# Performance work log

Hardware: AMD Instinct MI355X
Metric: run time of the kernel (lower is better)

Reference implementation:

```python
import jax, jax.numpy as jnp
import numpy as np

N = 50000
IN_DIM = 512
HID = 8
HEADS = 8
OUT_DIM = 7
E = 1600000
NEG_SLOPE = 0.2  # PyG GATConv default leaky_relu slope


def setup_inputs() -> dict:
    key = jax.random.key(0)
    ks = jax.random.split(key, 12)
    x = jax.random.normal(ks[0], (N, IN_DIM), dtype=jnp.float32)
    edge_index = jax.random.randint(ks[1], (2, E), 0, N, dtype=jnp.int64)
    s1 = 1.0 / np.sqrt(IN_DIM)
    s2 = 1.0 / np.sqrt(HID * HEADS)
    W1 = jax.random.normal(ks[2], (IN_DIM, HEADS * HID), dtype=jnp.float32) * s1
    att_src1 = jax.random.normal(ks[3], (HEADS, HID), dtype=jnp.float32) * s1
    att_dst1 = jax.random.normal(ks[4], (HEADS, HID), dtype=jnp.float32) * s1
    b1 = jnp.zeros((HEADS * HID,), dtype=jnp.float32)
    W2 = jax.random.normal(ks[5], (HEADS * HID, OUT_DIM), dtype=jnp.float32) * s2
    att_src2 = jax.random.normal(ks[6], (1, OUT_DIM), dtype=jnp.float32) * s2
    att_dst2 = jax.random.normal(ks[7], (1, OUT_DIM), dtype=jnp.float32) * s2
    b2 = jnp.zeros((OUT_DIM,), dtype=jnp.float32)
    return {"x": x, "edge_index": edge_index, "W1": W1, "att_src1": att_src1,
            "att_dst1": att_dst1, "b1": b1, "W2": W2, "att_src2": att_src2,
            "att_dst2": att_dst2, "b2": b2}


def _gat_layer(x, W, a_src, a_dst, b, src, dst, heads, out_ch, concat):
    n = x.shape[0]
    h = (x @ W).reshape(n, heads, out_ch)            # [N,H,C]
    asrc = jnp.sum(h * a_src, axis=-1)               # [N,H]
    adst = jnp.sum(h * a_dst, axis=-1)               # [N,H]
    e = jax.nn.leaky_relu(asrc[src] + adst[dst], NEG_SLOPE)   # [E,H]
    m = jax.ops.segment_max(e, dst, num_segments=n)           # segment softmax (stable)
    ex = jnp.exp(e - m[dst])
    s = jax.ops.segment_sum(ex, dst, num_segments=n)
    alpha = ex / jnp.maximum(s[dst], 1e-16)                   # [E,H]
    out = jax.ops.segment_sum(h[src] * alpha[..., None], dst, num_segments=n)  # [N,H,C]
    out = out.reshape(n, heads * out_ch) if concat else out.mean(axis=1)
    return out + b


def reference(x, edge_index, W1, att_src1, att_dst1, b1, W2, att_src2, att_dst2, b2):
    # add self-loops (PyG GATConv default add_self_loops=True)
    loop = jnp.arange(N, dtype=edge_index.dtype)
    src = jnp.concatenate([edge_index[0], loop])
    dst = jnp.concatenate([edge_index[1], loop])
    h = _gat_layer(x, W1, att_src1, att_dst1, b1, src, dst, HEADS, HID, True)
    h = jax.nn.elu(h)
    # dropout is identity at inference
    logits = _gat_layer(h, W2, att_src2, att_dst2, b2, src, dst, 1, OUT_DIM, False)
    return logits
```

## Files before the change

kernel.cpp:

```cpp
#include <hip/hip_runtime.h>
#include <hip/hip_bf16.h>

#define IN_DIM 512
#define HEADS 8
#define HID 8
#define OUT_DIM 7
#define NEG_SLOPE 0.2f

typedef __attribute__((ext_vector_type(8))) short short8b;
typedef __attribute__((ext_vector_type(4))) float f32x4;

#define BSHIFT 7
#define BMASK 127
#define K3_EPT 16

__device__ __forceinline__ unsigned short f2bf_rne(float f) {
    unsigned u = __float_as_uint(f);
    unsigned r = (u + 0x7FFFu + ((u >> 16) & 1u)) >> 16;
    return (unsigned short)r;
}
__device__ __forceinline__ float bf2f(unsigned short s) {
    return __uint_as_float((unsigned)s << 16);
}

__global__ __launch_bounds__(256) void prep_kernel(
    const float* __restrict__ W1, unsigned short* __restrict__ bhi,
    unsigned short* __restrict__ blo,
    const int* __restrict__ dst, int* __restrict__ bucketCounts, int E, int nbuck)
{
    __shared__ int cnt[512];
    int t = threadIdx.x;
    if (blockIdx.x < 128) {
        int i = blockIdx.x * 256 + t;
        int j = i & 7;
        int lane = (i >> 3) & 63;
        int T = (i >> 9) & 3;
        int chunk = i >> 11;
        int col = 16 * T + (lane & 15);
        int k = chunk * 32 + 8 * (lane >> 4) + j;
        float w = W1[k * 64 + col];
        unsigned u = __float_as_uint(w);
        unsigned hu = u & 0xFFFF0000u;
        float rem = w - __uint_as_float(hu);
        bhi[i] = (unsigned short)(hu >> 16);
        blo[i] = (unsigned short)(__float_as_uint(rem) >> 16);
    } else {
        int b = blockIdx.x - 128;
        cnt[t] = 0; cnt[t + 256] = 0;
        __syncthreads();
        int i = b * 256 + t;
        int stride = 512 * 256;
        for (; i < E; i += stride) atomicAdd(&cnt[dst[i] >> BSHIFT], 1);
        __syncthreads();
        if (t < nbuck && cnt[t]) atomicAdd(&bucketCounts[t], cnt[t]);
        int t2 = t + 256;
        if (t2 < nbuck && cnt[t2]) atomicAdd(&bucketCounts[t2], cnt[t2]);
    }
}

__global__ __launch_bounds__(512) void bucket_scan_kernel(
    const int* __restrict__ bucketCounts, int* __restrict__ bucketBase,
    int* __restrict__ bucketCursor, int nbuck)
{
    __shared__ int wsum[8];
    int t = threadIdx.x, lane = t & 63, w = t >> 6;
    int c = (t < nbuck) ? bucketCounts[t] : 0;
    int inc = c;
    #pragma unroll
    for (int d = 1; d < 64; d <<= 1) {
        int u = __shfl_up(inc, d);
        if (lane >= d) inc += u;
    }
    if (lane == 63) wsum[w] = inc;
    __syncthreads();
    if (t == 0) { int run = 0; for (int k = 0; k < 8; ++k) { int tmp = wsum[k]; wsum[k] = run; run += tmp; } }
    __syncthreads();
    int excl = inc - c + wsum[w];
    if (t < nbuck) { bucketBase[t] = excl; bucketCursor[t] = excl; }
    if (t == nbuck) bucketBase[t] = excl;
}

__global__ __launch_bounds__(256) void gemm1_coarse_kernel(
    const float* __restrict__ x,
    const unsigned short* __restrict__ bhi, const unsigned short* __restrict__ blo,
    const float* __restrict__ as1, const float* __restrict__ ad1,
    unsigned short* __restrict__ h1, float* __restrict__ asrc1, float* __restrict__ adst1,
    int n,
    const int* __restrict__ src, const int* __restrict__ dstv,
    int* __restrict__ bucketCursor, unsigned int* __restrict__ tmp, int E, int nGemm)
{
    __shared__ float lds[4][32][68];
    int t = threadIdx.x;

    if ((int)blockIdx.x >= nGemm) {
        int* cnt   = (int*)&lds[0][0][0];
        int* gbase = cnt + 512;
        cnt[t] = 0; cnt[t + 256] = 0;
        __syncthreads();
        int base = (blockIdx.x - nGemm) * (256 * K3_EPT);
        unsigned int pk[K3_EPT];
        unsigned int meta[K3_EPT];
        #pragma unroll
        for (int j = 0; j < K3_EPT; ++j) {
            int i = base + t + j * 256;
            if (i < E) {
                int d = dstv[i], s = src[i];
                int b = d >> BSHIFT;
                pk[j] = ((unsigned)s << 16) | (unsigned)(d & BMASK);
                int r = atomicAdd(&cnt[b], 1);
                meta[j] = ((unsigned)r << 9) | (unsigned)b;
            } else {
                meta[j] = 0xFFFFFFFFu; pk[j] = 0;
            }
        }
        __syncthreads();
        if (cnt[t] > 0) gbase[t] = atomicAdd(&bucketCursor[t], cnt[t]);
        int t2 = t + 256;
        if (cnt[t2] > 0) gbase[t2] = atomicAdd(&bucketCursor[t2], cnt[t2]);
        __syncthreads();
        #pragma unroll
        for (int j = 0; j < K3_EPT; ++j) {
            if (meta[j] != 0xFFFFFFFFu) {
                int b = meta[j] & 511;
                int r = meta[j] >> 9;
                tmp[gbase[b] + r] = pk[j];
            }
        }
        return;
    }

    int wave = t >> 6, l = t & 63;
    int il = l & 15, g = l >> 4;
    int r0 = blockIdx.x * 32;
    int kw = wave * 128;

    f32x4 acc[2][4] = {{{0.f,0.f,0.f,0.f},{0.f,0.f,0.f,0.f},{0.f,0.f,0.f,0.f},{0.f,0.f,0.f,0.f}},
                       {{0.f,0.f,0.f,0.f},{0.f,0.f,0.f,0.f},{0.f,0.f,0.f,0.f},{0.f,0.f,0.f,0.f}}};

    #pragma unroll
    for (int ph = 0; ph < 2; ++ph) {
        #pragma unroll
        for (int j = 0; j < 8; ++j) {
            int idx = j * 64 + l;
            int row = idx >> 4;
            int kq = idx & 15;
            int gr = r0 + row; if (gr >= n) gr = n - 1;
            float4 v = *(const float4*)(x + (size_t)gr * IN_DIM + kw + ph * 64 + kq * 4);
            *(float4*)(&lds[wave][row][kq * 4]) = v;
        }
        #pragma unroll
        for (int itp = 0; itp < 2; ++itp) {
            int it = ph * 2 + itp;
            int chunk = wave * 4 + it;
            const short8b* bh = (const short8b*)bhi + (size_t)(chunk * 4) * 64 + l;
            const short8b* bl = (const short8b*)blo + (size_t)(chunk * 4) * 64 + l;
            short8b Bh[4], Bl[4];
            #pragma unroll
            for (int T = 0; T < 4; ++T) { Bh[T] = bh[T * 64]; Bl[T] = bl[T * 64]; }
            #pragma unroll
            for (int rg = 0; rg < 2; ++rg) {
                float av[8];
                *(float4*)(&av[0]) = *(const float4*)(&lds[wave][rg * 16 + il][32 * itp + 8 * g]);
                *(float4*)(&av[4]) = *(const float4*)(&lds[wave][rg * 16 + il][32 * itp + 8 * g + 4]);
                short8b Ahi, Alo;
                #pragma unroll
                for (int j = 0; j < 8; ++j) {
                    unsigned u = __float_as_uint(av[j]);
                    unsigned hu = u & 0xFFFF0000u;
                    float rem = av[j] - __uint_as_float(hu);
                    Ahi[j] = (short)(hu >> 16);
                    Alo[j] = (short)(__float_as_uint(rem) >> 16);
                }
                #pragma unroll
                for (int T = 0; T < 4; ++T) {
                    acc[rg][T] = __builtin_amdgcn_mfma_f32_16x16x32_bf16(Alo, Bh[T], acc[rg][T], 0, 0, 0);
                    acc[rg][T] = __builtin_amdgcn_mfma_f32_16x16x32_bf16(Ahi, Bl[T], acc[rg][T], 0, 0, 0);
                    acc[rg][T] = __builtin_amdgcn_mfma_f32_16x16x32_bf16(Ahi, Bh[T], acc[rg][T], 0, 0, 0);
                }
            }
        }
    }

    #pragma unroll
    for (int rg = 0; rg < 2; ++rg)
        #pragma unroll
        for (int T = 0; T < 4; ++T)
            #pragma unroll
            for (int r = 0; r < 4; ++r)
                lds[wave][rg * 16 + 4 * g + r][16 * T + il] = acc[rg][T][r];
    __syncthreads();

    #pragma unroll
    for (int half = 0; half < 2; ++half) {
        int i = t + half * 256;
        int row = i >> 4, c0 = (i & 15) * 4;
        int grow = r0 + row;
        float v0 = lds[0][row][c0]     + lds[1][row][c0]     + lds[2][row][c0]     + lds[3][row][c0];
        float v1 = lds[0][row][c0 + 1] + lds[1][row][c0 + 1] + lds[2][row][c0 + 1] + lds[3][row][c0 + 1];
        float v2 = lds[0][row][c0 + 2] + lds[1][row][c0 + 2] + lds[2][row][c0 + 2] + lds[3][row][c0 + 2];
        float v3 = lds[0][row][c0 + 3] + lds[1][row][c0 + 3] + lds[2][row][c0 + 3] + lds[3][row][c0 + 3];
        float4 asv = *(const float4*)(as1 + c0);
        float4 adv = *(const float4*)(ad1 + c0);
        float pa = v0 * asv.x + v1 * asv.y + v2 * asv.z + v3 * asv.w;
        float pd = v0 * adv.x + v1 * adv.y + v2 * adv.z + v3 * adv.w;
        pa += __shfl_xor(pa, 1);
        pd += __shfl_xor(pd, 1);
        if (grow < n) {
            ushort4 hb;
            hb.x = f2bf_rne(v0); hb.y = f2bf_rne(v1);
            hb.z = f2bf_rne(v2); hb.w = f2bf_rne(v3);
            *(ushort4*)(h1 + (size_t)grow * 64 + c0) = hb;
            if ((t & 1) == 0) {
                int head = (i & 15) >> 1;
                asrc1[grow * 8 + head] = pa;
                adst1[grow * 8 + head] = pd;
            }
        }
    }
}

__global__ __launch_bounds__(256) void fine_scatter_kernel(
    const unsigned int* __restrict__ tmp, const int* __restrict__ bucketBase,
    int* __restrict__ csr, int* __restrict__ offsets, int* __restrict__ counts, int n)
{
    __shared__ int cnt[128];
    __shared__ int cur[128];
    __shared__ int wsum[2];
    int b = blockIdx.x;
    int t = threadIdx.x, lane = t & 63, w = t >> 6;
    int beg = bucketBase[b], end = bucketBase[b + 1];
    if (t < 128) cnt[t] = 0;
    __syncthreads();
    for (int i = beg + t; i < end; i += 256)
        atomicAdd(&cnt[tmp[i] & BMASK], 1);
    __syncthreads();
    if (t < 128) {
        int c = cnt[t];
        int inc = c;
        #pragma unroll
        for (int d = 1; d < 64; d <<= 1) {
            int u = __shfl_up(inc, d);
            if (lane >= d) inc += u;
        }
        if (lane == 63) wsum[w] = inc;
        __syncthreads();
        if (t == 0) { int r0_ = wsum[0]; wsum[0] = 0; wsum[1] = r0_; }
        __syncthreads();
        int excl = inc - c + wsum[w];
        int node = b * 128 + t;
        if (node < n) { offsets[node] = beg + excl; counts[node] = c; }
        cur[t] = excl;
    } else {
        __syncthreads(); __syncthreads();
    }
    __syncthreads();
    for (int i = beg + t; i < end; i += 256) {
        unsigned int p = tmp[i];
        int r = atomicAdd(&cur[p & BMASK], 1);
        csr[beg + r] = (int)(p >> 16);
    }
}

__global__ __launch_bounds__(256) void l1_edge_kernel(
    const int* __restrict__ offsets, const int* __restrict__ counts,
    const int* __restrict__ csr,
    const float* __restrict__ asrc1, const float* __restrict__ adst1,
    const unsigned short* __restrict__ h1, const float* __restrict__ b1,
    const float* __restrict__ W2, const float* __restrict__ as2,
    const float* __restrict__ ad2,
    float* __restrict__ h2, float* __restrict__ asrc2, float* __restrict__ adst2,
    int n)
{
    __shared__ float w2t[8][64];
    __shared__ float s_as2[8], s_ad2[8], s_b1[64];
    __shared__ int csr_s[4][64];
    int t = threadIdx.x;
    if (t < 64) {
        #pragma unroll
        for (int j = 0; j < OUT_DIM; ++j) w2t[j][t] = W2[t * OUT_DIM + j];
        s_b1[t] = b1[t];
        if (t < OUT_DIM) { s_as2[t] = as2[t]; s_ad2[t] = ad2[t]; }
    }
    __syncthreads();

    int lane = t & 63;
    int nl = t >> 6;
    int node = blockIdx.x * 4 + nl;
    if (node >= n) return;
    int beg = offsets[node];
    int deg = counts[node];
    int q = lane >> 4;
    int il = lane & 15;
    int c0 = il * 4;
    int head = il >> 1;
    float adv = adst1[node * 8 + head];

    if (lane < deg) csr_s[nl][lane] = csr[beg + lane];
    int deg_r = deg < 64 ? deg : 64;
    const int* cs = &csr_s[nl][0];

    float4 acc = make_float4(0.f, 0.f, 0.f, 0.f);
    float ssum = 0.f;
    if (q == 0) {
        float e = asrc1[node * 8 + head] + adv;
        e = e > 0.f ? e : NEG_SLOPE * e;
        float p = __expf(e);
        ushort4 hu = *(const ushort4*)(h1 + (size_t)node * 64 + c0);
        acc.x = p * bf2f(hu.x); acc.y = p * bf2f(hu.y);
        acc.z = p * bf2f(hu.z); acc.w = p * bf2f(hu.w);
        ssum = p;
    }
    int j = q;
    for (; j + 12 < deg_r; j += 16) {
        int s0 = cs[j];
        int s1 = cs[j + 4];
        int s2 = cs[j + 8];
        int s3 = cs[j + 12];
        float a0 = asrc1[s0 * 8 + head], a1 = asrc1[s1 * 8 + head];
        float a2 = asrc1[s2 * 8 + head], a3 = asrc1[s3 * 8 + head];
        ushort4 g0 = *(const ushort4*)(h1 + (size_t)s0 * 64 + c0);
        ushort4 g1 = *(const ushort4*)(h1 + (size_t)s1 * 64 + c0);
        ushort4 g2 = *(const ushort4*)(h1 + (size_t)s2 * 64 + c0);
        ushort4 g3 = *(const ushort4*)(h1 + (size_t)s3 * 64 + c0);
        float e0 = a0 + adv; e0 = e0 > 0.f ? e0 : NEG_SLOPE * e0;
        float e1 = a1 + adv; e1 = e1 > 0.f ? e1 : NEG_SLOPE * e1;
        float e2 = a2 + adv; e2 = e2 > 0.f ? e2 : NEG_SLOPE * e2;
        float e3 = a3 + adv; e3 = e3 > 0.f ? e3 : NEG_SLOPE * e3;
        float p0 = __expf(e0), p1 = __expf(e1);
        float p2 = __expf(e2), p3 = __expf(e3);
        acc.x = fmaf(p0, bf2f(g0.x), acc.x); acc.y = fmaf(p0, bf2f(g0.y), acc.y);
        acc.z = fmaf(p0, bf2f(g0.z), acc.z); acc.w = fmaf(p0, bf2f(g0.w), acc.w);
        acc.x = fmaf(p1, bf2f(g1.x), acc.x); acc.y = fmaf(p1, bf2f(g1.y), acc.y);
        acc.z = fmaf(p1, bf2f(g1.z), acc.z); acc.w = fmaf(p1, bf2f(g1.w), acc.w);
        acc.x = fmaf(p2, bf2f(g2.x), acc.x); acc.y = fmaf(p2, bf2f(g2.y), acc.y);
        acc.z = fmaf(p2, bf2f(g2.z), acc.z); acc.w = fmaf(p2, bf2f(g2.w), acc.w);
        acc.x = fmaf(p3, bf2f(g3.x), acc.x); acc.y = fmaf(p3, bf2f(g3.y), acc.y);
        acc.z = fmaf(p3, bf2f(g3.z), acc.z); acc.w = fmaf(p3, bf2f(g3.w), acc.w);
        ssum += (p0 + p1) + (p2 + p3);
    }
    for (; j < deg_r; j += 4) {
        int sn = cs[j];
        float a = asrc1[sn * 8 + head];
        ushort4 g = *(const ushort4*)(h1 + (size_t)sn * 64 + c0);
        float e = a + adv; e = e > 0.f ? e : NEG_SLOPE * e;
        float p = __expf(e);
        acc.x = fmaf(p, bf2f(g.x), acc.x); acc.y = fmaf(p, bf2f(g.y), acc.y);
        acc.z = fmaf(p, bf2f(g.z), acc.z); acc.w = fmaf(p, bf2f(g.w), acc.w);
        ssum += p;
    }
    for (; j < deg; j += 4) {
        int sn = csr[beg + j];
        float a = asrc1[sn * 8 + head];
        ushort4 g = *(const ushort4*)(h1 + (size_t)sn * 64 + c0);
        float e = a + adv; e = e > 0.f ? e : NEG_SLOPE * e;
        float p = __expf(e);
        acc.x = fmaf(p, bf2f(g.x), acc.x); acc.y = fmaf(p, bf2f(g.y), acc.y);
        acc.z = fmaf(p, bf2f(g.z), acc.z); acc.w = fmaf(p, bf2f(g.w), acc.w);
        ssum += p;
    }
    acc.x += __shfl_xor(acc.x, 16); acc.x += __shfl_xor(acc.x, 32);
    acc.y += __shfl_xor(acc.y, 16); acc.y += __shfl_xor(acc.y, 32);
    acc.z += __shfl_xor(acc.z, 16); acc.z += __shfl_xor(acc.z, 32);
    acc.w += __shfl_xor(acc.w, 16); acc.w += __shfl_xor(acc.w, 32);
    ssum  += __shfl_xor(ssum, 16);  ssum  += __shfl_xor(ssum, 32);
    float inv = 1.f / fmaxf(ssum, 1e-16f);

    float4 bv = *(const float4*)(&s_b1[c0]);
    float v0 = acc.x * inv + bv.x;
    float v1 = acc.y * inv + bv.y;
    float v2 = acc.z * inv + bv.z;
    float v3 = acc.w * inv + bv.w;
    v0 = v0 > 0.f ? v0 : __expf(v0) - 1.f;
    v1 = v1 > 0.f ? v1 : __expf(v1) - 1.f;
    v2 = v2 > 0.f ? v2 : __expf(v2) - 1.f;
    v3 = v3 > 0.f ? v3 : __expf(v3) - 1.f;

    float hj[OUT_DIM];
    #pragma unroll
    for (int jj = 0; jj < OUT_DIM; ++jj) {
        float4 wv = *(const float4*)(&w2t[jj][c0]);
        float p = v0 * wv.x + v1 * wv.y + v2 * wv.z + v3 * wv.w;
        p += __shfl_xor(p, 1);
        p += __shfl_xor(p, 2);
        p += __shfl_xor(p, 4);
        p += __shfl_xor(p, 8);
        hj[jj] = p;
    }
    float a_s = 0.f, a_d = 0.f;
    #pragma unroll
    for (int jj = 0; jj < OUT_DIM; ++jj) { a_s += hj[jj] * s_as2[jj]; a_d += hj[jj] * s_ad2[jj]; }
    if (lane < 8) h2[node * 8 + lane] = (lane < OUT_DIM) ? hj[lane] : 0.f;
    if (lane == 0) { asrc2[node] = a_s; adst2[node] = a_d; }
}

__global__ __launch_bounds__(256) void l2_edge_kernel(
    const int* __restrict__ offsets, const int* __restrict__ counts,
    const int* __restrict__ csr,
    const float* __restrict__ asrc2, const float* __restrict__ adst2,
    const float* __restrict__ h2, const float* __restrict__ b2,
    float* __restrict__ out, int n)
{
    int t = threadIdx.x, lane = t & 63;
    int node = blockIdx.x * 4 + (t >> 6);
    if (node >= n) return;
    int beg = offsets[node];
    int deg = counts[node];
    float adv = adst2[node];

    int c = lane & 7, slot = lane >> 3;
    float acc = 0.f, ssum = 0.f;
    if (slot == 0) {
        float e = asrc2[node] + adv;
        e = e > 0.f ? e : NEG_SLOPE * e;
        float p = __expf(e);
        acc = p * h2[node * 8 + c];
        ssum = p;
    }
    int j = slot;
    for (; j + 8 < deg; j += 16) {
        int s0 = csr[beg + j], s1 = csr[beg + j + 8];
        float a0 = asrc2[s0], a1 = asrc2[s1];
        float g0 = h2[s0 * 8 + c], g1 = h2[s1 * 8 + c];
        float e0 = a0 + adv; e0 = e0 > 0.f ? e0 : NEG_SLOPE * e0;
        float e1 = a1 + adv; e1 = e1 > 0.f ? e1 : NEG_SLOPE * e1;
        float p0 = __expf(e0), p1 = __expf(e1);
        acc = fmaf(p0, g0, acc); acc = fmaf(p1, g1, acc);
        ssum += p0 + p1;
    }
    for (; j < deg; j += 8) {
        int sn = csr[beg + j];
        float e = asrc2[sn] + adv;
        e = e > 0.f ? e : NEG_SLOPE * e;
        float p = __expf(e);
        acc = fmaf(p, h2[sn * 8 + c], acc);
        ssum += p;
    }
    acc  += __shfl_xor(acc, 8);  acc  += __shfl_xor(acc, 16);  acc  += __shfl_xor(acc, 32);
    ssum += __shfl_xor(ssum, 8); ssum += __shfl_xor(ssum, 16); ssum += __shfl_xor(ssum, 32);
    float inv = 1.f / fmaxf(ssum, 1e-16f);
    if (lane < OUT_DIM) out[(size_t)node * OUT_DIM + lane] = acc * inv + b2[lane];
}

static inline size_t rup256(size_t x) { return (x + 255) & ~(size_t)255; }

extern "C" void kernel_launch(void* const* d_in, const int* in_sizes, int n_in,
                              void* d_out, int out_size, void* d_ws, size_t ws_size,
                              hipStream_t stream)
{
    int n = in_sizes[0] / IN_DIM;
    int E = in_sizes[1] / 2;
    int nbuck = (n + BMASK) >> BSHIFT;
    int nCoarse = (E + 256 * K3_EPT - 1) / (256 * K3_EPT);
    int nGemm = (n + 31) / 32;

    const float* x   = (const float*)d_in[0];
    const int*   ei  = (const int*)d_in[1];
    const int*   srcv = ei;
    const int*   dstv = ei + E;
    const float* W1  = (const float*)d_in[2];
    const float* as1 = (const float*)d_in[3];
    const float* ad1 = (const float*)d_in[4];
    const float* b1  = (const float*)d_in[5];
    const float* W2  = (const float*)d_in[6];
    const float* as2 = (const float*)d_in[7];
    const float* ad2 = (const float*)d_in[8];
    const float* b2  = (const float*)d_in[9];
    float* out = (float*)d_out;

    char* p = (char*)d_ws;
    auto alloc = [&](size_t bytes) { char* q = p; p += rup256(bytes); return (void*)q; };
    unsigned short* h1 = (unsigned short*)alloc((size_t)n * 64 * 2);
    float* asrc1   = (float*)alloc((size_t)n * 8 * 4);
    float* adst1   = (float*)alloc((size_t)n * 8 * 4);
    float* h2      = (float*)alloc((size_t)n * 8 * 4);
    float* asrc2   = (float*)alloc((size_t)n * 4);
    float* adst2   = (float*)alloc((size_t)n * 4);
    int*   counts  = (int*)alloc((size_t)n * 4);
    int*   offsets = (int*)alloc(((size_t)n + 1) * 4);
    int*   csr     = (int*)alloc((size_t)E * 4);
    unsigned int* tmp = (unsigned int*)alloc((size_t)E * 4);
    int*   bucketCounts = (int*)alloc(512 * 4);
    int*   bucketBase   = (int*)alloc(513 * 4);
    int*   bucketCursor = (int*)alloc(512 * 4);
    unsigned short* bhi = (unsigned short*)alloc((size_t)IN_DIM * 64 * 2);
    unsigned short* blo = (unsigned short*)alloc((size_t)IN_DIM * 64 * 2);

    hipMemsetAsync(bucketCounts, 0, 512 * 4, stream);
    prep_kernel<<<128 + 512, 256, 0, stream>>>(W1, bhi, blo, dstv, bucketCounts, E, nbuck);
    bucket_scan_kernel<<<1, 512, 0, stream>>>(bucketCounts, bucketBase, bucketCursor, nbuck);
    gemm1_coarse_kernel<<<nGemm + nCoarse, 256, 0, stream>>>(
        x, bhi, blo, as1, ad1, h1, asrc1, adst1, n,
        srcv, dstv, bucketCursor, tmp, E, nGemm);
    fine_scatter_kernel<<<nbuck, 256, 0, stream>>>(
        tmp, bucketBase, csr, offsets, counts, n);
    l1_edge_kernel<<<(n + 3) / 4, 256, 0, stream>>>(
        offsets, counts, csr, asrc1, adst1, h1, b1, W2, as2, ad2, h2, asrc2, adst2, n);
    l2_edge_kernel<<<(n + 3) / 4, 256, 0, stream>>>(
        offsets, counts, csr, asrc2, adst2, h2, b2, out, n);
}
```

Before: 143.1 us.

## Replace global atomic bucket cursors with per-block histogram and prefix scan

```diff
diff --git a/kernel.cpp b/kernel.cpp
--- a/kernel.cpp
+++ b/kernel.cpp
@@ -26,7 +26,7 @@
 __global__ __launch_bounds__(256) void prep_kernel(
     const float* __restrict__ W1, unsigned short* __restrict__ bhi,
     unsigned short* __restrict__ blo,
-    const int* __restrict__ dst, int* __restrict__ bucketCounts, int E, int nbuck)
+    const int* __restrict__ dst, int* __restrict__ blockCnt, int E)
 {
     __shared__ int cnt[512];
     int t = threadIdx.x;
@@ -45,26 +45,29 @@
         bhi[i] = (unsigned short)(hu >> 16);
         blo[i] = (unsigned short)(__float_as_uint(rem) >> 16);
     } else {
-        int b = blockIdx.x - 128;
+        int hb = blockIdx.x - 128;
         cnt[t] = 0; cnt[t + 256] = 0;
         __syncthreads();
-        int i = b * 256 + t;
-        int stride = 512 * 256;
-        for (; i < E; i += stride) atomicAdd(&cnt[dst[i] >> BSHIFT], 1);
-        __syncthreads();
-        if (t < nbuck && cnt[t]) atomicAdd(&bucketCounts[t], cnt[t]);
-        int t2 = t + 256;
-        if (t2 < nbuck && cnt[t2]) atomicAdd(&bucketCounts[t2], cnt[t2]);
-    }
-}
-
-__global__ __launch_bounds__(512) void bucket_scan_kernel(
-    const int* __restrict__ bucketCounts, int* __restrict__ bucketBase,
-    int* __restrict__ bucketCursor, int nbuck)
+        int base = hb * (256 * K3_EPT);
+        #pragma unroll
+        for (int j = 0; j < K3_EPT; ++j) {
+            int i = base + t + j * 256;
+            if (i < E) atomicAdd(&cnt[dst[i] >> BSHIFT], 1);
+        }
+        __syncthreads();
+        blockCnt[hb * 512 + t] = cnt[t];
+        blockCnt[hb * 512 + 256 + t] = cnt[t + 256];
+    }
+}
+
+__global__ __launch_bounds__(512) void blk_scan_kernel(
+    const int* __restrict__ blockCnt, int* __restrict__ blockOfs,
+    int* __restrict__ bucketTotal, int nCoarse)
 {
     __shared__ int wsum[8];
+    int b = blockIdx.x;
     int t = threadIdx.x, lane = t & 63, w = t >> 6;
-    int c = (t < nbuck) ? bucketCounts[t] : 0;
+    int c = (t < nCoarse) ? blockCnt[t * 512 + b] : 0;
     int inc = c;
     #pragma unroll
     for (int d = 1; d < 64; d <<= 1) {
@@ -76,7 +79,28 @@
     if (t == 0) { int run = 0; for (int k = 0; k < 8; ++k) { int tmp = wsum[k]; wsum[k] = run; run += tmp; } }
     __syncthreads();
     int excl = inc - c + wsum[w];
-    if (t < nbuck) { bucketBase[t] = excl; bucketCursor[t] = excl; }
+    if (t < nCoarse) blockOfs[t * 512 + b] = excl;
+    if (t == nCoarse - 1) bucketTotal[b] = excl + c;
+}
+
+__global__ __launch_bounds__(512) void bucket_scan_kernel(
+    const int* __restrict__ bucketTotal, int* __restrict__ bucketBase, int nbuck)
+{
+    __shared__ int wsum[8];
+    int t = threadIdx.x, lane = t & 63, w = t >> 6;
+    int c = (t < nbuck) ? bucketTotal[t] : 0;
+    int inc = c;
+    #pragma unroll
+    for (int d = 1; d < 64; d <<= 1) {
+        int u = __shfl_up(inc, d);
+        if (lane >= d) inc += u;
+    }
+    if (lane == 63) wsum[w] = inc;
+    __syncthreads();
+    if (t == 0) { int run = 0; for (int k = 0; k < 8; ++k) { int tmp = wsum[k]; wsum[k] = run; run += tmp; } }
+    __syncthreads();
+    int excl = inc - c + wsum[w];
+    if (t < nbuck) bucketBase[t] = excl;
     if (t == nbuck) bucketBase[t] = excl;
 }
 
@@ -87,17 +111,19 @@
     unsigned short* __restrict__ h1, float* __restrict__ asrc1, float* __restrict__ adst1,
     int n,
     const int* __restrict__ src, const int* __restrict__ dstv,
-    int* __restrict__ bucketCursor, unsigned int* __restrict__ tmp, int E, int nGemm)
+    const int* __restrict__ bucketBase, const int* __restrict__ blockOfs,
+    unsigned int* __restrict__ tmp, int E, int nGemm)
 {
     __shared__ float lds[4][32][68];
     int t = threadIdx.x;
 
     if ((int)blockIdx.x >= nGemm) {
+        int cb = blockIdx.x - nGemm;
         int* cnt   = (int*)&lds[0][0][0];
         int* gbase = cnt + 512;
         cnt[t] = 0; cnt[t + 256] = 0;
         __syncthreads();
-        int base = (blockIdx.x - nGemm) * (256 * K3_EPT);
+        int base = cb * (256 * K3_EPT);
         unsigned int pk[K3_EPT];
         unsigned int meta[K3_EPT];
         #pragma unroll
@@ -114,9 +140,8 @@
             }
         }
         __syncthreads();
-        if (cnt[t] > 0) gbase[t] = atomicAdd(&bucketCursor[t], cnt[t]);
-        int t2 = t + 256;
-        if (cnt[t2] > 0) gbase[t2] = atomicAdd(&bucketCursor[t2], cnt[t2]);
+        gbase[t]       = bucketBase[t]       + blockOfs[cb * 512 + t];
+        gbase[t + 256] = bucketBase[t + 256] + blockOfs[cb * 512 + t + 256];
         __syncthreads();
         #pragma unroll
         for (int j = 0; j < K3_EPT; ++j) {
@@ -479,18 +504,19 @@
     int*   offsets = (int*)alloc(((size_t)n + 1) * 4);
     int*   csr     = (int*)alloc((size_t)E * 4);
     unsigned int* tmp = (unsigned int*)alloc((size_t)E * 4);
-    int*   bucketCounts = (int*)alloc(512 * 4);
-    int*   bucketBase   = (int*)alloc(513 * 4);
-    int*   bucketCursor = (int*)alloc(512 * 4);
+    int*   blockCnt = (int*)alloc((size_t)nCoarse * 512 * 4);
+    int*   blockOfs = (int*)alloc((size_t)nCoarse * 512 * 4);
+    int*   bucketTotal = (int*)alloc(512 * 4);
+    int*   bucketBase  = (int*)alloc(513 * 4);
     unsigned short* bhi = (unsigned short*)alloc((size_t)IN_DIM * 64 * 2);
     unsigned short* blo = (unsigned short*)alloc((size_t)IN_DIM * 64 * 2);
 
-    hipMemsetAsync(bucketCounts, 0, 512 * 4, stream);
-    prep_kernel<<<128 + 512, 256, 0, stream>>>(W1, bhi, blo, dstv, bucketCounts, E, nbuck);
-    bucket_scan_kernel<<<1, 512, 0, stream>>>(bucketCounts, bucketBase, bucketCursor, nbuck);
+    prep_kernel<<<128 + nCoarse, 256, 0, stream>>>(W1, bhi, blo, dstv, blockCnt, E);
+    blk_scan_kernel<<<nbuck, 512, 0, stream>>>(blockCnt, blockOfs, bucketTotal, nCoarse);
+    bucket_scan_kernel<<<1, 512, 0, stream>>>(bucketTotal, bucketBase, nbuck);
     gemm1_coarse_kernel<<<nGemm + nCoarse, 256, 0, stream>>>(
         x, bhi, blo, as1, ad1, h1, asrc1, adst1, n,
-        srcv, dstv, bucketCursor, tmp, E, nGemm);
+        srcv, dstv, bucketBase, blockOfs, tmp, E, nGemm);
     fine_scatter_kernel<<<nbuck, 256, 0, stream>>>(
         tmp, bucketBase, csr, offsets, counts, n);
     l1_edge_kernel<<<(n + 3) / 4, 256, 0, stream>>>(
```

Result: faster. 130.1 us (-9.1%).
